# Kernel tuning notes

Measured on AMD Instinct MI355X. Metric: run time of the kernel, lower is better.

Reference implementation:

```python
import jax, jax.numpy as jnp
import numpy as np

B, T, D, S = 64, 512, 1024, 1024


def setup_inputs() -> dict:
    key = jax.random.key(0)
    k1, k2, k3, k4 = jax.random.split(key, 4)
    a = jax.random.normal(k1, (B, T, D), dtype=jnp.float32)
    s_prev = jax.random.normal(k2, (B, S), dtype=jnp.float32)
    # Dense(10, tanh) over concat dim D+S; Dense(1, relu). Glorot-ish scale.
    W1 = jax.random.normal(k3, (D + S, 10), dtype=jnp.float32) * (1.0 / np.sqrt(D + S))
    b1 = jnp.zeros((10,), dtype=jnp.float32)
    W2 = jax.random.normal(k4, (10, 1), dtype=jnp.float32) * (1.0 / np.sqrt(10))
    b2 = jnp.zeros((1,), dtype=jnp.float32)
    return {"a": a, "s_prev": s_prev, "W1": W1, "b1": b1, "W2": W2, "b2": b2}


def reference(a, s_prev, W1, b1, W2, b2):
    # RepeatVector: [B,S] -> [B,T,S]
    s_rep = jnp.broadcast_to(s_prev[:, None, :], (a.shape[0], a.shape[1], s_prev.shape[-1]))
    x = jnp.concatenate([a, s_rep], axis=-1)               # [B,T,D+S]
    h = jnp.tanh(jnp.einsum('btc,cu->btu', x, W1) + b1)    # [B,T,10]
    e = jax.nn.relu(jnp.einsum('btu,uo->bto', h, W2) + b2) # [B,T,1]
    attention_score = jax.nn.softmax(e, axis=1)            # softmax over time
    context_vector = jnp.sum(attention_score * a, axis=1, keepdims=True)  # [B,1,D]
    return context_vector, attention_score
```

## Files before the change

kernel.cpp:

```cpp
#include <hip/hip_runtime.h>
#include <stdint.h>

#define B_ 64
#define T_ 512
#define D_ 1024
#define S_ 1024
#define U_ 10

typedef float f32x2 __attribute__((ext_vector_type(2)));
typedef float f32x4 __attribute__((ext_vector_type(4)));

static constexpr int WS_PMZ = 0;
static constexpr int WS_E   = 1024;
static constexpr int WS_PV  = 33792;
static constexpr int WS_C   = 33792 + 512 * 1024;

template <int CTRL>
__device__ __forceinline__ float dpp_add(float x) {
    int yi = __builtin_amdgcn_update_dpp(0, __float_as_int(x), CTRL, 0xf, 0xf, true);
    return x + __int_as_float(yi);
}
template <int CTRL>
__device__ __forceinline__ float dpp_max(float x) {
    int yi = __builtin_amdgcn_update_dpp(__float_as_int(-1e30f), __float_as_int(x),
                                         CTRL, 0xf, 0xf, true);
    return fmaxf(x, __int_as_float(yi));
}

__device__ __forceinline__ float wave_sum63(float x) {
    x = dpp_add<0x111>(x);
    x = dpp_add<0x112>(x);
    x = dpp_add<0x114>(x);
    x = dpp_add<0x118>(x);
    x = dpp_add<0x142>(x);
    x = dpp_add<0x143>(x);
    return x;
}
__device__ __forceinline__ float wave_sum_uniform(float x) {
    return __int_as_float(__builtin_amdgcn_readlane(__float_as_int(wave_sum63(x)), 63));
}
__device__ __forceinline__ float wave_max_uniform(float x) {
    x = dpp_max<0x111>(x);
    x = dpp_max<0x112>(x);
    x = dpp_max<0x114>(x);
    x = dpp_max<0x118>(x);
    x = dpp_max<0x142>(x);
    x = dpp_max<0x143>(x);
    return __int_as_float(__builtin_amdgcn_readlane(__float_as_int(x), 63));
}

__device__ __forceinline__ f32x2 pk_fma(f32x2 a, f32x2 b, f32x2 c) {
#if __has_builtin(__builtin_elementwise_fma)
    return __builtin_elementwise_fma(a, b, c);
#else
    return a * b + c;
#endif
}

__global__ __launch_bounds__(256) void k0_prep(const float* __restrict__ s_prev,
                                               const float* __restrict__ W1,
                                               const float* __restrict__ b1,
                                               float* __restrict__ ws) {
    const int b    = blockIdx.x;
    const int tid  = threadIdx.x;
    const int wave = tid >> 6;
    const int lane = tid & 63;

    f32x2 acc2[5];
#pragma unroll
    for (int h = 0; h < 5; h++) acc2[h] = f32x2{0.f, 0.f};

    const f32x4 s4 = *(const f32x4*)(s_prev + b * S_ + tid * 4);
    const float sv[4] = {s4.x, s4.y, s4.z, s4.w};
#pragma unroll
    for (int i = 0; i < 4; i++) {
        const float* wp = W1 + (size_t)(D_ + tid * 4 + i) * U_;
        const f32x2 svv = f32x2{sv[i], sv[i]};
#pragma unroll
        for (int h = 0; h < 5; h++)
            acc2[h] = pk_fma(svv, *(const f32x2*)(wp + 2 * h), acc2[h]);
    }

    __shared__ float red[4][U_];
    const float vals[U_] = {acc2[0].x, acc2[0].y, acc2[1].x, acc2[1].y, acc2[2].x,
                            acc2[2].y, acc2[3].x, acc2[3].y, acc2[4].x, acc2[4].y};
#pragma unroll
    for (int u = 0; u < U_; u++) {
        float s = wave_sum63(vals[u]);
        if (lane == 63) red[wave][u] = s;
    }
    __syncthreads();
    if (tid < U_)
        ws[WS_C + b * U_ + tid] =
            red[0][tid] + red[1][tid] + red[2][tid] + red[3][tid] + b1[tid];
}

__global__ __launch_bounds__(256, 2) void k1_main(const float* __restrict__ a,
                                                  const float* __restrict__ W1,
                                                  const float* __restrict__ W2,
                                                  const float* __restrict__ b2,
                                                  float* __restrict__ ws) {
    const int blk  = blockIdx.x;
    const int b    = blk >> 3;
    const int p    = blk & 7;
    const int tid  = threadIdx.x;
    const int wave = tid >> 6;
    const int lane = tid & 63;

    __shared__ __align__(16) float stg[4][2][2048];
    __shared__ float pmat[4][64][U_];
    __shared__ float wbuf[64];

    const int t0 = p * 64;
    const size_t arow0 = (size_t)(b * T_ + t0) * D_;
    const int dof0 = __builtin_amdgcn_readfirstlane(wave * 256);

    const int rsub = lane >> 3;
    const int slog = (lane & 7) ^ rsub;

    auto stage = [&](int buf, int c) {
        const float* base = a + arow0 + (size_t)(dof0 + c * 32 + slog * 4);
        float* dst = &stg[wave][buf][0];
#pragma unroll
        for (int k = 0; k < 8; k++) {
            const float* src = base + (size_t)(8 * k + rsub) * D_;
            __builtin_amdgcn_global_load_lds(
                (const __attribute__((address_space(1))) uint32_t*)src,
                (__attribute__((address_space(3))) uint32_t*)(dst + k * 256),
                16, 0, 0);
        }
    };

    f32x2 acc2[5];
#pragma unroll
    for (int h = 0; h < 5; h++) acc2[h] = f32x2{0.f, 0.f};

    stage(0, 0);

#pragma unroll 1
    for (int c = 0; c < 8; c++) {
        if (c < 7) {
            stage((c + 1) & 1, c + 1);
            asm volatile("s_waitcnt vmcnt(8)" ::: "memory");
        } else {
            asm volatile("s_waitcnt vmcnt(0)" ::: "memory");
        }
        __builtin_amdgcn_sched_barrier(0);

        const float* tb    = &stg[wave][c & 1][lane * 32];
        const float* wbase = W1 + (size_t)(dof0 + c * 32) * U_;
#pragma unroll
        for (int j = 0; j < 8; j++) {
            const f32x4 av = *(const f32x4*)(tb + ((j ^ (lane & 7)) << 2));
            const float* wd = wbase + j * 4 * U_;
            const float avv[4] = {av.x, av.y, av.z, av.w};
#pragma unroll
            for (int i = 0; i < 4; i++) {
                const f32x2 ax = f32x2{avv[i], avv[i]};
#pragma unroll
                for (int h = 0; h < 5; h++)
                    acc2[h] = pk_fma(ax, *(const f32x2*)(wd + i * U_ + 2 * h), acc2[h]);
            }
        }
    }

#pragma unroll
    for (int h = 0; h < 5; h++)
        *(f32x2*)(&pmat[wave][lane][2 * h]) = acc2[h];
    __syncthreads();

    if (wave == 0) {
        const float* cb = ws + WS_C + b * U_;
        float e = b2[0];
#pragma unroll
        for (int u = 0; u < U_; u++) {
            float x = pmat[0][lane][u] + pmat[1][lane][u] + pmat[2][lane][u] +
                      pmat[3][lane][u] + cb[u];
            float ex = exp2f(x * 2.8853900817779268f);
            float th = 1.f - 2.f * __builtin_amdgcn_rcpf(ex + 1.f);
            e += th * W2[u];
        }
        e = fmaxf(e, 0.f);
        ws[WS_E + b * T_ + t0 + lane] = e;

        const float mb = wave_max_uniform(e);
        const float w  = exp2f((e - mb) * 1.4426950408889634f);
        const float Zb = wave_sum_uniform(w);
        wbuf[lane] = w;
        if (lane == 0) { ws[WS_PMZ + blk * 2] = mb; ws[WS_PMZ + blk * 2 + 1] = Zb; }
    }
    __syncthreads();

    f32x4 v0 = f32x4{0.f, 0.f, 0.f, 0.f};
    f32x4 v1 = f32x4{0.f, 0.f, 0.f, 0.f};
    const float* ap = a + arow0 + tid * 4;
#pragma unroll 8
    for (int t = 0; t < 64; t += 2) {
        v0 += wbuf[t]     * *(const f32x4*)(ap + (size_t)t * D_);
        v1 += wbuf[t + 1] * *(const f32x4*)(ap + (size_t)(t + 1) * D_);
    }
    ((f32x4*)(ws + WS_PV))[blk * 256 + tid] = v0 + v1;
}

__global__ __launch_bounds__(256) void k2_final(const float* __restrict__ ws,
                                                float* __restrict__ out) {
    const int b = blockIdx.x;
    const int tid = threadIdx.x;

    float pm[8], pz[8];
    float mb = -1e30f;
#pragma unroll
    for (int p = 0; p < 8; p++) {
        pm[p] = ws[WS_PMZ + (b * 8 + p) * 2];
        pz[p] = ws[WS_PMZ + (b * 8 + p) * 2 + 1];
        mb = fmaxf(mb, pm[p]);
    }
    float f[8], Z = 0.f;
#pragma unroll
    for (int p = 0; p < 8; p++) { f[p] = __expf(pm[p] - mb); Z += f[p] * pz[p]; }
    const float rz = 1.f / Z;

    f32x4 o = f32x4{0.f, 0.f, 0.f, 0.f};
#pragma unroll
    for (int p = 0; p < 8; p++) {
        f32x4 t = ((const f32x4*)(ws + WS_PV))[(b * 8 + p) * 256 + tid];
        o += f[p] * t;
    }
    o *= rz;
    ((f32x4*)out)[b * 256 + tid] = o;

    for (int t = tid; t < T_; t += 256) {
        out[B_ * D_ + b * T_ + t] = __expf(ws[WS_E + b * T_ + t] - mb) * rz;
    }
}

extern "C" void kernel_launch(void* const* d_in, const int* in_sizes, int n_in,
                              void* d_out, int out_size, void* d_ws, size_t ws_size,
                              hipStream_t stream) {
    const float* a      = (const float*)d_in[0];
    const float* s_prev = (const float*)d_in[1];
    const float* W1     = (const float*)d_in[2];
    const float* b1     = (const float*)d_in[3];
    const float* W2     = (const float*)d_in[4];
    const float* b2     = (const float*)d_in[5];
    float* out = (float*)d_out;
    float* ws  = (float*)d_ws;

    k0_prep<<<dim3(B_), dim3(256), 0, stream>>>(s_prev, W1, b1, ws);
    k1_main<<<dim3(B_ * 8), dim3(256), 0, stream>>>(a, W1, W2, b2, ws);
    k2_final<<<dim3(B_), dim3(256), 0, stream>>>(ws, out);
}
```

Baseline: 245.6 us.

## Stage W1 slice in LDS and halve k1 block to two waves

The main kernel now copies the first D rows of W1 (40 KB) into shared memory once per block and reads weights from LDS instead of global/scalar loads. The block drops from four to two waves, so each wave covers 512 columns over 16 chunks, and the partial-sum scratch reuses the staging buffer. The weighted-sum pass has each thread handle 8 columns. This trades global weight reads for an extra 40 KB LDS copy per block, with fewer waves per block and possibly lower occupancy and latency hiding.

```diff
diff --git a/kernel.cpp b/kernel.cpp
--- a/kernel.cpp
+++ b/kernel.cpp
@@ -95,11 +95,11 @@
             red[0][tid] + red[1][tid] + red[2][tid] + red[3][tid] + b1[tid];
 }
 
-__global__ __launch_bounds__(256, 2) void k1_main(const float* __restrict__ a,
-                                                  const float* __restrict__ W1,
-                                                  const float* __restrict__ W2,
-                                                  const float* __restrict__ b2,
-                                                  float* __restrict__ ws) {
+__global__ __launch_bounds__(128) void k1_main(const float* __restrict__ a,
+                                               const float* __restrict__ W1,
+                                               const float* __restrict__ W2,
+                                               const float* __restrict__ b2,
+                                               float* __restrict__ ws) {
     const int blk  = blockIdx.x;
     const int b    = blk >> 3;
     const int p    = blk & 7;
@@ -107,13 +107,14 @@
     const int wave = tid >> 6;
     const int lane = tid & 63;
 
-    __shared__ __align__(16) float stg[4][2][2048];
-    __shared__ float pmat[4][64][U_];
+    __shared__ __align__(16) float w1s[D_ * U_];
+    __shared__ __align__(16) float stg[2][2][2048];
     __shared__ float wbuf[64];
+    float* const pmat = &stg[0][0][0];
 
     const int t0 = p * 64;
     const size_t arow0 = (size_t)(b * T_ + t0) * D_;
-    const int dof0 = __builtin_amdgcn_readfirstlane(wave * 256);
+    const int dof0 = __builtin_amdgcn_readfirstlane(wave * 512);
 
     const int rsub = lane >> 3;
     const int slog = (lane & 7) ^ rsub;
@@ -131,15 +132,22 @@
         }
     };
 
+    stage(0, 0);
+    {
+        const f32x4* wsrc = (const f32x4*)W1;
+        f32x4* wdst = (f32x4*)w1s;
+#pragma unroll
+        for (int q = 0; q < 20; q++) wdst[tid + 128 * q] = wsrc[tid + 128 * q];
+    }
+    __syncthreads();
+
     f32x2 acc2[5];
 #pragma unroll
     for (int h = 0; h < 5; h++) acc2[h] = f32x2{0.f, 0.f};
 
-    stage(0, 0);
-
 #pragma unroll 1
-    for (int c = 0; c < 8; c++) {
-        if (c < 7) {
+    for (int c = 0; c < 16; c++) {
+        if (c < 15) {
             stage((c + 1) & 1, c + 1);
             asm volatile("s_waitcnt vmcnt(8)" ::: "memory");
         } else {
@@ -148,7 +156,7 @@
         __builtin_amdgcn_sched_barrier(0);
 
         const float* tb    = &stg[wave][c & 1][lane * 32];
-        const float* wbase = W1 + (size_t)(dof0 + c * 32) * U_;
+        const float* wbase = w1s + (size_t)(dof0 + c * 32) * U_;
 #pragma unroll
         for (int j = 0; j < 8; j++) {
             const f32x4 av = *(const f32x4*)(tb + ((j ^ (lane & 7)) << 2));
@@ -164,9 +172,10 @@
         }
     }
 
+    __syncthreads();
 #pragma unroll
     for (int h = 0; h < 5; h++)
-        *(f32x2*)(&pmat[wave][lane][2 * h]) = acc2[h];
+        *(f32x2*)(&pmat[(wave * 64 + lane) * U_ + 2 * h]) = acc2[h];
     __syncthreads();
 
     if (wave == 0) {
@@ -174,8 +183,7 @@
         float e = b2[0];
 #pragma unroll
         for (int u = 0; u < U_; u++) {
-            float x = pmat[0][lane][u] + pmat[1][lane][u] + pmat[2][lane][u] +
-                      pmat[3][lane][u] + cb[u];
+            float x = pmat[lane * U_ + u] + pmat[(64 + lane) * U_ + u] + cb[u];
             float ex = exp2f(x * 2.8853900817779268f);
             float th = 1.f - 2.f * __builtin_amdgcn_rcpf(ex + 1.f);
             e += th * W2[u];
@@ -193,13 +201,15 @@
 
     f32x4 v0 = f32x4{0.f, 0.f, 0.f, 0.f};
     f32x4 v1 = f32x4{0.f, 0.f, 0.f, 0.f};
-    const float* ap = a + arow0 + tid * 4;
+    const float* ap = a + arow0 + tid * 8;
 #pragma unroll 8
-    for (int t = 0; t < 64; t += 2) {
-        v0 += wbuf[t]     * *(const f32x4*)(ap + (size_t)t * D_);
-        v1 += wbuf[t + 1] * *(const f32x4*)(ap + (size_t)(t + 1) * D_);
-    }
-    ((f32x4*)(ws + WS_PV))[blk * 256 + tid] = v0 + v1;
+    for (int t = 0; t < 64; t++) {
+        const float wt = wbuf[t];
+        v0 += wt * *(const f32x4*)(ap + (size_t)t * D_);
+        v1 += wt * *(const f32x4*)(ap + (size_t)t * D_ + 4);
+    }
+    ((f32x4*)(ws + WS_PV))[blk * 256 + tid * 2]     = v0;
+    ((f32x4*)(ws + WS_PV))[blk * 256 + tid * 2 + 1] = v1;
 }
 
 __global__ __launch_bounds__(256) void k2_final(const float* __restrict__ ws,
@@ -247,6 +257,6 @@
     float* ws  = (float*)d_ws;
 
     k0_prep<<<dim3(B_), dim3(256), 0, stream>>>(s_prev, W1, b1, ws);
-    k1_main<<<dim3(B_ * 8), dim3(256), 0, stream>>>(a, W1, W2, b2, ws);
+    k1_main<<<dim3(B_ * 8), dim3(128), 0, stream>>>(a, W1, W2, b2, ws);
     k2_final<<<dim3(B_), dim3(256), 0, stream>>>(ws, out);
 }
```

New measurement: 221.1 us. -10.0%, faster.

## Restructure main kernel: W1 in LDS, per-wave row tiles, register prefetch

Applied to the files above, without the earlier changes.

The main kernel now stages the first D rows of W1 into padded LDS once per block. Each wave handles 16 time rows, with 8 lanes splitting each row's D dimension, instead of splitting D across waves and staging `a` through LDS with async global-to-LDS loads. Partial dot products are reduced with DPP within 8-lane groups, and softmax stats are computed per wave then merged in LDS. This removes the cross-wave pmat reduction and the serial single-wave epilogue, and replaces per-FMA global reads of W1 with LDS reads. In exchange it uses register prefetch of `a`, which raises register pressure, and it re-reads `a` for the weighted sum.

```diff
diff --git a/kernel.cpp b/kernel.cpp
--- a/kernel.cpp
+++ b/kernel.cpp
@@ -22,8 +22,7 @@
 }
 template <int CTRL>
 __device__ __forceinline__ float dpp_max(float x) {
-    int yi = __builtin_amdgcn_update_dpp(__float_as_int(-1e30f), __float_as_int(x),
-                                         CTRL, 0xf, 0xf, true);
+    int yi = __builtin_amdgcn_update_dpp(0, __float_as_int(x), CTRL, 0xf, 0xf, true);
     return fmaxf(x, __int_as_float(yi));
 }
 
@@ -36,17 +35,12 @@
     x = dpp_add<0x143>(x);
     return x;
 }
-__device__ __forceinline__ float wave_sum_uniform(float x) {
-    return __int_as_float(__builtin_amdgcn_readlane(__float_as_int(wave_sum63(x)), 63));
-}
-__device__ __forceinline__ float wave_max_uniform(float x) {
-    x = dpp_max<0x111>(x);
-    x = dpp_max<0x112>(x);
-    x = dpp_max<0x114>(x);
-    x = dpp_max<0x118>(x);
-    x = dpp_max<0x142>(x);
-    x = dpp_max<0x143>(x);
-    return __int_as_float(__builtin_amdgcn_readlane(__float_as_int(x), 63));
+
+__device__ __forceinline__ float rdlane15(float x) {
+    return __int_as_float(__builtin_amdgcn_readlane(__float_as_int(x), 15));
+}
+__device__ __forceinline__ float uload(const float* p) {
+    return __int_as_float(__builtin_amdgcn_readfirstlane(__float_as_int(*p)));
 }
 
 __device__ __forceinline__ f32x2 pk_fma(f32x2 a, f32x2 b, f32x2 c) {
@@ -107,99 +101,155 @@
     const int wave = tid >> 6;
     const int lane = tid & 63;
 
-    __shared__ __align__(16) float stg[4][2][2048];
-    __shared__ float pmat[4][64][U_];
-    __shared__ float wbuf[64];
-
-    const int t0 = p * 64;
-    const size_t arow0 = (size_t)(b * T_ + t0) * D_;
-    const int dof0 = __builtin_amdgcn_readfirstlane(wave * 256);
-
-    const int rsub = lane >> 3;
-    const int slog = (lane & 7) ^ rsub;
-
-    auto stage = [&](int buf, int c) {
-        const float* base = a + arow0 + (size_t)(dof0 + c * 32 + slog * 4);
-        float* dst = &stg[wave][buf][0];
-#pragma unroll
-        for (int k = 0; k < 8; k++) {
-            const float* src = base + (size_t)(8 * k + rsub) * D_;
-            __builtin_amdgcn_global_load_lds(
-                (const __attribute__((address_space(1))) uint32_t*)src,
-                (__attribute__((address_space(3))) uint32_t*)(dst + k * 256),
-                16, 0, 0);
-        }
-    };
-
-    f32x2 acc2[5];
-#pragma unroll
-    for (int h = 0; h < 5; h++) acc2[h] = f32x2{0.f, 0.f};
-
-    stage(0, 0);
+    __shared__ __align__(16) float w1s[10256];
+    __shared__ float esh[4][16];
+    __shared__ float wsh[4][16];
+    __shared__ float mzs[4][2];
+
+#pragma unroll
+    for (int r = 0; r < 4; r++) {
+        const int d = r * 256 + tid;
+        const float* wp = W1 + (size_t)d * U_;
+        const int fb = d * U_ + 2 * (d >> 7);
+#pragma unroll
+        for (int h = 0; h < 5; h++)
+            *(f32x2*)(&w1s[fb + 2 * h]) = *(const f32x2*)(wp + 2 * h);
+    }
+
+    float c[U_], w2v[U_];
+    {
+        const float* cb = ws + WS_C + b * U_;
+#pragma unroll
+        for (int u = 0; u < U_; u++) c[u] = uload(cb + u);
+#pragma unroll
+        for (int u = 0; u < U_; u++) w2v[u] = uload(W2 + u);
+    }
+    const float b2s = uload(b2);
+    __syncthreads();
+
+    const int tt = lane >> 3;
+    const int g  = lane & 7;
+    const int t0w = p * 64 + wave * 16;
+
+    const float* aA = a + (size_t)(b * T_ + t0w + tt) * D_ + g * 128;
+    const float* aB = aA + (size_t)8 * D_;
+    const int wb = g * 1282;
+
+    f32x2 accA[5], accB[5];
+#pragma unroll
+    for (int h = 0; h < 5; h++) { accA[h] = f32x2{0.f, 0.f}; accB[h] = f32x2{0.f, 0.f}; }
+
+    f32x4 rA[4], rB[4];
+#pragma unroll
+    for (int q = 0; q < 4; q++) {
+        rA[q] = *(const f32x4*)(aA + q * 4);
+        rB[q] = *(const f32x4*)(aB + q * 4);
+    }
 
 #pragma unroll 1
-    for (int c = 0; c < 8; c++) {
-        if (c < 7) {
-            stage((c + 1) & 1, c + 1);
-            asm volatile("s_waitcnt vmcnt(8)" ::: "memory");
-        } else {
-            asm volatile("s_waitcnt vmcnt(0)" ::: "memory");
-        }
-        __builtin_amdgcn_sched_barrier(0);
-
-        const float* tb    = &stg[wave][c & 1][lane * 32];
-        const float* wbase = W1 + (size_t)(dof0 + c * 32) * U_;
-#pragma unroll
-        for (int j = 0; j < 8; j++) {
-            const f32x4 av = *(const f32x4*)(tb + ((j ^ (lane & 7)) << 2));
-            const float* wd = wbase + j * 4 * U_;
-            const float avv[4] = {av.x, av.y, av.z, av.w};
+    for (int j = 0; j < 32; j += 4) {
+#pragma unroll
+        for (int q = 0; q < 4; q++) {
+            const f32x4 vA = rA[q], vB = rB[q];
+            if (j + 4 + q < 32) {
+                rA[q] = *(const f32x4*)(aA + (j + 4 + q) * 4);
+                rB[q] = *(const f32x4*)(aB + (j + 4 + q) * 4);
+            }
+            const int fbase = wb + (j + q) * 40;
+            const float aAv[4] = {vA.x, vA.y, vA.z, vA.w};
+            const float aBv[4] = {vB.x, vB.y, vB.z, vB.w};
 #pragma unroll
             for (int i = 0; i < 4; i++) {
-                const f32x2 ax = f32x2{avv[i], avv[i]};
-#pragma unroll
-                for (int h = 0; h < 5; h++)
-                    acc2[h] = pk_fma(ax, *(const f32x2*)(wd + i * U_ + 2 * h), acc2[h]);
+                const f32x2* wp = (const f32x2*)&w1s[fbase + i * 10];
+                const f32x2 va = f32x2{aAv[i], aAv[i]};
+                const f32x2 vb = f32x2{aBv[i], aBv[i]};
+#pragma unroll
+                for (int h = 0; h < 5; h++) {
+                    const f32x2 wv = wp[h];
+                    accA[h] = pk_fma(va, wv, accA[h]);
+                    accB[h] = pk_fma(vb, wv, accB[h]);
+                }
             }
         }
     }
 
-#pragma unroll
-    for (int h = 0; h < 5; h++)
-        *(f32x2*)(&pmat[wave][lane][2 * h]) = acc2[h];
+    float xsA[U_] = {accA[0].x, accA[0].y, accA[1].x, accA[1].y, accA[2].x,
+                     accA[2].y, accA[3].x, accA[3].y, accA[4].x, accA[4].y};
+    float xsB[U_] = {accB[0].x, accB[0].y, accB[1].x, accB[1].y, accB[2].x,
+                     accB[2].y, accB[3].x, accB[3].y, accB[4].x, accB[4].y};
+#pragma unroll
+    for (int u = 0; u < U_; u++) {
+        xsA[u] = dpp_add<0x114>(dpp_add<0x112>(dpp_add<0x111>(xsA[u])));
+        xsB[u] = dpp_add<0x114>(dpp_add<0x112>(dpp_add<0x111>(xsB[u])));
+    }
+
+    if (g == 7) {
+        float eA = b2s, eB = b2s;
+#pragma unroll
+        for (int u = 0; u < U_; u++) {
+            float xA = xsA[u] + c[u];
+            float xB = xsB[u] + c[u];
+            float exA = exp2f(xA * 2.8853900817779268f);
+            float exB = exp2f(xB * 2.8853900817779268f);
+            eA += (1.f - 2.f * __builtin_amdgcn_rcpf(exA + 1.f)) * w2v[u];
+            eB += (1.f - 2.f * __builtin_amdgcn_rcpf(exB + 1.f)) * w2v[u];
+        }
+        eA = fmaxf(eA, 0.f);
+        eB = fmaxf(eB, 0.f);
+        esh[wave][tt]     = eA;
+        esh[wave][tt + 8] = eB;
+        ws[WS_E + b * T_ + t0w + tt]     = eA;
+        ws[WS_E + b * T_ + t0w + tt + 8] = eB;
+    }
+
+    const float el = esh[wave][lane & 15];
+    float mx = dpp_max<0x118>(dpp_max<0x114>(dpp_max<0x112>(dpp_max<0x111>(el))));
+    const float m = rdlane15(mx);
+    const float w_l = exp2f((el - m) * 1.4426950408889634f);
+    float zt = dpp_add<0x118>(dpp_add<0x114>(dpp_add<0x112>(dpp_add<0x111>(w_l))));
+    const float Z = rdlane15(zt);
+    if (lane < 16) wsh[wave][lane] = w_l;
+    if (lane == 0) { mzs[wave][0] = m; mzs[wave][1] = Z; }
+
+    f32x2 v2[4][2];
+#pragma unroll
+    for (int k = 0; k < 4; k++) { v2[k][0] = f32x2{0.f, 0.f}; v2[k][1] = f32x2{0.f, 0.f}; }
+    const float* abase = a + (size_t)(b * T_ + t0w) * D_ + lane * 4;
+#pragma unroll 4
+    for (int t = 0; t < 16; t++) {
+        const float wt = wsh[wave][t];
+        const f32x2 wv = f32x2{wt, wt};
+        const float* ar = abase + (size_t)t * D_;
+#pragma unroll
+        for (int k = 0; k < 4; k++) {
+            const f32x4 av = *(const f32x4*)(ar + k * 256);
+            v2[k][0] = pk_fma(wv, av.lo, v2[k][0]);
+            v2[k][1] = pk_fma(wv, av.hi, v2[k][1]);
+        }
+    }
+
     __syncthreads();
-
-    if (wave == 0) {
-        const float* cb = ws + WS_C + b * U_;
-        float e = b2[0];
-#pragma unroll
-        for (int u = 0; u < U_; u++) {
-            float x = pmat[0][lane][u] + pmat[1][lane][u] + pmat[2][lane][u] +
-                      pmat[3][lane][u] + cb[u];
-            float ex = exp2f(x * 2.8853900817779268f);
-            float th = 1.f - 2.f * __builtin_amdgcn_rcpf(ex + 1.f);
-            e += th * W2[u];
-        }
-        e = fmaxf(e, 0.f);
-        ws[WS_E + b * T_ + t0 + lane] = e;
-
-        const float mb = wave_max_uniform(e);
-        const float w  = exp2f((e - mb) * 1.4426950408889634f);
-        const float Zb = wave_sum_uniform(w);
-        wbuf[lane] = w;
-        if (lane == 0) { ws[WS_PMZ + blk * 2] = mb; ws[WS_PMZ + blk * 2 + 1] = Zb; }
+    f32x4* vs4 = (f32x4*)&w1s[0];
+#pragma unroll
+    for (int k = 0; k < 4; k++) {
+        f32x4 o;
+        o.lo = v2[k][0];
+        o.hi = v2[k][1];
+        vs4[wave * 256 + k * 64 + lane] = o;
     }
     __syncthreads();
 
-    f32x4 v0 = f32x4{0.f, 0.f, 0.f, 0.f};
-    f32x4 v1 = f32x4{0.f, 0.f, 0.f, 0.f};
-    const float* ap = a + arow0 + tid * 4;
-#pragma unroll 8
-    for (int t = 0; t < 64; t += 2) {
-        v0 += wbuf[t]     * *(const f32x4*)(ap + (size_t)t * D_);
-        v1 += wbuf[t + 1] * *(const f32x4*)(ap + (size_t)(t + 1) * D_);
-    }
-    ((f32x4*)(ws + WS_PV))[blk * 256 + tid] = v0 + v1;
+    float m0 = mzs[0][0], m1 = mzs[1][0], m2 = mzs[2][0], m3 = mzs[3][0];
+    float mb = fmaxf(fmaxf(m0, m1), fmaxf(m2, m3));
+    float f0 = __expf(m0 - mb), f1 = __expf(m1 - mb);
+    float f2 = __expf(m2 - mb), f3 = __expf(m3 - mb);
+    float Zb = f0 * mzs[0][1] + f1 * mzs[1][1] + f2 * mzs[2][1] + f3 * mzs[3][1];
+
+    f32x4 t0v = vs4[0 * 256 + tid], t1v = vs4[1 * 256 + tid];
+    f32x4 t2v = vs4[2 * 256 + tid], t3v = vs4[3 * 256 + tid];
+    f32x4 o = f0 * t0v + f1 * t1v + f2 * t2v + f3 * t3v;
+    ((f32x4*)(ws + WS_PV))[blk * 256 + tid] = o;
+    if (tid == 0) { ws[WS_PMZ + blk * 2] = mb; ws[WS_PMZ + blk * 2 + 1] = Zb; }
 }
 
 __global__ __launch_bounds__(256) void k2_final(const float* __restrict__ ws,
```

Result: faster. 230.6 us (-6.1%).
